# Kernel optimization log

Hardware: AMD Instinct MI355X
Metric: run time of the kernel (lower is better)

The kernel has to match this reference:

```python
import jax, jax.numpy as jnp
import numpy as np

B, L, H, NH = 2, 256, 512, 8
DH = H // NH
MAXLEN = 256           # module's max_seq_len; pe index offset
PE_ROWS = 2 * MAXLEN + 1


def _lin(x, W, b):
    # torch nn.Linear convention: y = x @ W.T + b
    return x @ W.T + b


def setup_inputs() -> dict:
    rng = jax.random.key(0)
    ks = jax.random.split(rng, 24)
    s = 0.02
    inp = {
        "key": jax.random.normal(ks[0], (B, L, H), jnp.float32),
        "query": jax.random.normal(ks[1], (B, L, H), jnp.float32),
        "value": jax.random.normal(ks[2], (B, L, H), jnp.float32),
        # learned params
        "pe": jax.random.normal(ks[3], (PE_ROWS, H), jnp.float32) * s,
        "Wf": jax.random.normal(ks[4], (H, 4 * H), jnp.float32) * s,
        "bf": jnp.zeros((H,), jnp.float32),
        "Wk": jax.random.normal(ks[5], (H, H), jnp.float32) * s,
        "bk": jnp.zeros((H,), jnp.float32),
        "Wq": jax.random.normal(ks[6], (H, H), jnp.float32) * s,
        "bq": jnp.zeros((H,), jnp.float32),
        "Wv": jax.random.normal(ks[7], (H, H), jnp.float32) * s,
        "bv": jnp.zeros((H,), jnp.float32),
        "Wr": jax.random.normal(ks[8], (H, H), jnp.float32) * s,
        "br": jnp.zeros((H,), jnp.float32),
        "Wo": jax.random.normal(ks[9], (H, H), jnp.float32) * s,  # ff_final
        "bo": jnp.zeros((H,), jnp.float32),
        "u": jax.random.normal(ks[10], (NH, DH), jnp.float32) * s,
        "v": jax.random.normal(ks[11], (NH, DH), jnp.float32) * s,
        # int inputs
        "seq_len": jax.random.randint(ks[12], (B,), 100, 200).astype(jnp.int64),
        "lex_num": jax.random.randint(ks[13], (B,), 0, 50).astype(jnp.int64),
    }
    pos_s = jax.random.randint(ks[14], (B, L), 0, 250)
    pos_e = pos_s + jax.random.randint(ks[15], (B, L), 0, 5)
    inp["pos_s"] = pos_s.astype(jnp.int64)
    inp["pos_e"] = pos_e.astype(jnp.int64)
    return inp


def reference(key, query, value, pe, Wf, bf, Wk, bk, Wq, bq, Wv, bv, Wr, br,
              Wo, bo, u, v, seq_len, lex_num, pos_s, pos_e):
    b, l, _ = key.shape
    # four relative position matrices [B, L, L]
    pos_ss = pos_s[:, :, None] - pos_s[:, None, :]
    pos_se = pos_s[:, :, None] - pos_e[:, None, :]
    pos_es = pos_e[:, :, None] - pos_s[:, None, :]
    pos_ee = pos_e[:, :, None] - pos_e[:, None, :]
    # gather pe embeddings, each [B, L, L, H]
    pe_ss = pe[pos_ss + MAXLEN]
    pe_se = pe[pos_se + MAXLEN]
    pe_es = pe[pos_es + MAXLEN]
    pe_ee = pe[pos_ee + MAXLEN]
    pe_4 = jnp.concatenate([pe_ss, pe_se, pe_es, pe_ee], axis=-1)  # [B,L,L,4H]
    rel = jax.nn.relu(_lin(pe_4, Wf, bf))                          # 'ff' fusion -> [B,L,L,H]

    q = _lin(query, Wq, bq).reshape(b, l, NH, DH).transpose(0, 2, 1, 3)  # [B,nh,L,dh]
    k = _lin(key, Wk, bk).reshape(b, l, NH, DH).transpose(0, 2, 1, 3)
    val = _lin(value, Wv, bv).reshape(b, l, NH, DH).transpose(0, 2, 1, 3)
    rel = _lin(rel, Wr, br).reshape(b, l, l, NH, DH)               # [B,L,L,nh,dh]

    A = jnp.einsum('bhid,bhjd->bhij', q, k)
    B_ = jnp.einsum('bhid,bijhd->bhij', q, rel)
    C = jnp.einsum('hd,bhjd->bhj', u, k)[:, :, None, :]
    D = jnp.einsum('hd,bijhd->bhij', v, rel)

    score = (A + B_ + C + D) / np.float32(np.sqrt(DH))
    total_len = seq_len + lex_num                                   # [B]
    mask = (jnp.arange(l)[None, :] < total_len[:, None])[:, None, None, :]
    score = jnp.where(mask, score, jnp.float32(-1e15))
    attn = jax.nn.softmax(score, axis=-1)
    out = jnp.einsum('bhij,bhjd->bhid', attn, val)                  # [B,nh,L,dh]
    out = out.transpose(0, 2, 1, 3).reshape(b, l, H)
    return _lin(out, Wo, bo)
```

## Files before the change

### kernel.cpp

```cpp
#include <hip/hip_runtime.h>
#include <hip/hip_bf16.h>

typedef unsigned short USHORT;
typedef long long LL;
typedef short s8v __attribute__((ext_vector_type(8)));
typedef float f32x4 __attribute__((ext_vector_type(4)));


__device__ __forceinline__ float bf2f(USHORT u) {
  union { unsigned int i; float f; } v; v.i = ((unsigned int)u) << 16; return v.f;
}
__device__ __forceinline__ USHORT f2bf(float f) {
  unsigned int x = __float_as_uint(f);
  unsigned int r = (x + 0x7fffu + ((x >> 16) & 1u)) >> 16;
  return (USHORT)r;
}

struct PrepArgs {
  const void* fsrc[18]; USHORT* fdst[18]; int fn[18];
  const void* wr_src; USHORT* wrT;
  const void* isrc[4]; int* idst[4];
};

__global__ __launch_bounds__(256) void prep_k(PrepArgs a, const void* qraw, int* flags) {
  __shared__ int s_w;
  const int t = threadIdx.x;
  if (t == 0) s_w = 0;
  __syncthreads();
  const USHORT* qb = (const USHORT*)qraw;
  int wild = 0;
  for (int c = t; c < 512; c += 256) {
    float x = bf2f(qb[c]);
    if (!(fabsf(x) <= 1024.0f)) wild = 1;
  }
  if (wild) atomicAdd(&s_w, 1);
  __syncthreads();
  const int f = (s_w == 0) ? 1 : 0;

  const int y = blockIdx.y;
  if (y < 18) {
    const int n = a.fn[y];
    const USHORT* sb = (const USHORT*)a.fsrc[y];
    const float* sf = (const float*)a.fsrc[y];
    USHORT* d = a.fdst[y];
    for (int idx = blockIdx.x * 256 + t; idx < n; idx += gridDim.x * 256)
      d[idx] = f ? sb[idx] : f2bf(sf[idx]);
  } else if (y == 18) {
    const USHORT* sb = (const USHORT*)a.wr_src;
    const float* sf = (const float*)a.wr_src;
    for (int idx = blockIdx.x * 256 + t; idx < 262144; idx += gridDim.x * 256) {
      const int e = idx >> 9, dd = idx & 511;
      const int s = dd * 512 + e;
      a.wrT[idx] = f ? sb[s] : f2bf(sf[s]);
    }
  } else if (blockIdx.x == 0) {
    if (t == 0) flags[0] = f;
    const int fi = (((const int*)a.isrc[0])[1] == 0) ? 1 : 0;
    if (t < 2) {
      a.idst[0][t] = fi ? (int)((const LL*)a.isrc[0])[t] : ((const int*)a.isrc[0])[t];
      a.idst[1][t] = fi ? (int)((const LL*)a.isrc[1])[t] : ((const int*)a.isrc[1])[t];
    }
    for (int c = t; c < 512; c += 256) {
      a.idst[2][c] = fi ? (int)((const LL*)a.isrc[2])[c] : ((const int*)a.isrc[2])[c];
      a.idst[3][c] = fi ? (int)((const LL*)a.isrc[3])[c] : ((const int*)a.isrc[3])[c];
    }
  }
}

struct GDesc {
  const USHORT* A; const USHORT* W; const USHORT* bias;
  void* out;
  int M, N, K, lda, ldw, koff, mode;
};
struct GArgs { GDesc d[32]; };

__global__ __launch_bounds__(256) void gemm2_k(GArgs ga, const int* __restrict__ flags) {
  const GDesc de = ga.d[blockIdx.z];
  const int row0 = blockIdx.y * 64, col0 = blockIdx.x * 64;
  if (row0 >= de.M || col0 >= de.N) return;
  const int wave = threadIdx.x >> 6, lane = threadIdx.x & 63;
  const int mrow = row0 + wave * 16 + (lane & 15);
  const int kq = (lane >> 4) * 8;
  const bool mok = (mrow < de.M);
  const USHORT* ar = de.A + (long)(mok ? mrow : 0) * de.lda + kq;
  const int nc = col0 + (lane & 15);
  const USHORT* w0p = de.W + (long)(nc +  0) * de.ldw + de.koff + kq;
  const USHORT* w1p = de.W + (long)(nc + 16) * de.ldw + de.koff + kq;
  const USHORT* w2p = de.W + (long)(nc + 32) * de.ldw + de.koff + kq;
  const USHORT* w3p = de.W + (long)(nc + 48) * de.ldw + de.koff + kq;

  f32x4 acc[4] = {};
#pragma unroll 4
  for (int k0 = 0; k0 < de.K; k0 += 32) {
    s8v a = *(const s8v*)(ar + k0);
    s8v wv0 = *(const s8v*)(w0p + k0);
    s8v wv1 = *(const s8v*)(w1p + k0);
    s8v wv2 = *(const s8v*)(w2p + k0);
    s8v wv3 = *(const s8v*)(w3p + k0);
    acc[0] = __builtin_amdgcn_mfma_f32_16x16x32_bf16(a, wv0, acc[0], 0, 0, 0);
    acc[1] = __builtin_amdgcn_mfma_f32_16x16x32_bf16(a, wv1, acc[1], 0, 0, 0);
    acc[2] = __builtin_amdgcn_mfma_f32_16x16x32_bf16(a, wv2, acc[2], 0, 0, 0);
    acc[3] = __builtin_amdgcn_mfma_f32_16x16x32_bf16(a, wv3, acc[3], 0, 0, 0);
  }

  const int obf = (de.mode == 2) ? flags[0] : (de.mode == 1);
  const int mbase = row0 + wave * 16 + (lane >> 4) * 4;
#pragma unroll
  for (int nt = 0; nt < 4; nt++) {
    const int n = col0 + nt * 16 + (lane & 15);
    const float bias = de.bias ? bf2f(de.bias[n]) : 0.f;
#pragma unroll
    for (int r = 0; r < 4; r++) {
      const int m = mbase + r;
      if (m >= de.M) continue;
      const float vo = acc[nt][r] + bias;
      const long off = (long)m * de.N + n;
      if (obf) ((USHORT*)de.out)[off] = f2bf(vo);
      else     ((float*)de.out)[off] = vo;
    }
  }
}

__global__ __launch_bounds__(256) void qvb2_k(
    const float* __restrict__ qp, const float* __restrict__ kp,
    const USHORT* __restrict__ u_bf, const USHORT* __restrict__ v_bf,
    const USHORT* __restrict__ br_bf,
    USHORT* __restrict__ qv, USHORT* __restrict__ qu, USHORT* __restrict__ kb,
    float* __restrict__ cbv_buf)
{
  const int idx = blockIdx.x * 256 + threadIdx.x;
  const int d = idx & 63, i = (idx >> 6) & 255, h = (idx >> 14) & 7, b = idx >> 17;
  const int hd = h * 64 + d;
  const long row = (long)(b * 256 + i) * 512 + hd;
  const float q = qp[row];
  const float qpv = q + bf2f(v_bf[hd]);
  qv[idx] = f2bf(qpv);
  qu[idx] = f2bf(q + bf2f(u_bf[hd]));
  kb[idx] = f2bf(kp[row]);
  float s = qpv * bf2f(br_bf[hd]);
#pragma unroll
  for (int off = 32; off > 0; off >>= 1) s += __shfl_xor(s, off);
  if ((threadIdx.x & 63) == 0) cbv_buf[idx >> 6] = s;
}

__global__ __launch_bounds__(256) void score2_k(
    const USHORT* __restrict__ Ptab_bf, const float* __restrict__ S_AC,
    const float* __restrict__ cbv_buf, const USHORT* __restrict__ wbuf_bf,
    const float* __restrict__ vp,
    const int* __restrict__ seq_len, const int* __restrict__ lex_num,
    const int* __restrict__ pos_s, const int* __restrict__ pos_e,
    USHORT* __restrict__ out_pre_bf)
{
  __shared__ float Sm[8 * 257];
  __shared__ int psj_s[256], pej_s[256];
  __shared__ float red4[4];

  const int i = blockIdx.x, b = blockIdx.y, t = threadIdx.x;
  const int wave = t >> 6, lane = t & 63;
  const int n = lane & 15, q = lane >> 4;
  int tl = seq_len[b] + lex_num[b];
  tl = min(max(tl, 1), 256);
  const int psi = pos_s[b * 256 + i];
  const int pei = pos_e[b * 256 + i];

  if (t < 256) { psj_s[t] = pos_s[b * 256 + t]; pej_s[t] = pos_e[b * 256 + t]; }

  s8v wf[16];
  if (n < 8) {
    const USHORT* wr = wbuf_bf + ((long)((b * 8 + n) * 256 + i)) * 512 + q * 8;
#pragma unroll
    for (int kk = 0; kk < 16; kk++) wf[kk] = *(const s8v*)(wr + kk * 32);
  } else {
#pragma unroll
    for (int kk = 0; kk < 16; kk++) wf[kk] = (s8v){0, 0, 0, 0, 0, 0, 0, 0};
  }
  __syncthreads();

  const USHORT* P1 = Ptab_bf;
  const USHORT* P2 = Ptab_bf + 513l * 512;
  const USHORT* P3 = Ptab_bf + 2l * 513 * 512;
  const USHORT* P4 = Ptab_bf + 3l * 513 * 512;

  const int ntiles = (tl + 15) >> 4;
  for (int jt = wave; jt < ntiles; jt += 4) {
    const int j0 = jt * 16;
    const int j = j0 + n;
    const int psj = psj_s[j], pej = pej_s[j];
    const long i0 = (long)min(max(psi - psj + 256, 0), 512) * 512 + q * 8;
    const long i1 = (long)min(max(psi - pej + 256, 0), 512) * 512 + q * 8;
    const long i2 = (long)min(max(pei - psj + 256, 0), 512) * 512 + q * 8;
    const long i3 = (long)min(max(pei - pej + 256, 0), 512) * 512 + q * 8;
    f32x4 acc = {0.f, 0.f, 0.f, 0.f};
#pragma unroll
    for (int kk = 0; kk < 16; kk++) {
      const int e0 = kk * 32;
      s8v a0 = *(const s8v*)(P1 + i0 + e0);
      s8v a1 = *(const s8v*)(P2 + i1 + e0);
      s8v a2 = *(const s8v*)(P3 + i2 + e0);
      s8v a3 = *(const s8v*)(P4 + i3 + e0);
      s8v af;
#pragma unroll
      for (int x = 0; x < 8; x++) {
        const float fs = bf2f((USHORT)a0[x]) + bf2f((USHORT)a1[x]) +
                         bf2f((USHORT)a2[x]) + bf2f((USHORT)a3[x]);
        af[x] = (short)f2bf(fmaxf(fs, 0.f));
      }
      acc = __builtin_amdgcn_mfma_f32_16x16x32_bf16(af, wf[kk], acc, 0, 0, 0);
    }
    if (n < 8) {
      const long base = (long)(b * 8 + n) * 256 + i;
      const float cb = cbv_buf[base];
      const float4 sac = *(const float4*)(S_AC + base * 256 + j0 + q * 4);
      const float* sacp = (const float*)&sac;
#pragma unroll
      for (int r = 0; r < 4; r++)
        Sm[n * 257 + j0 + q * 4 + r] = (acc[r] + sacp[r] + cb) * 0.125f;
    }
  }
  __syncthreads();

  for (int h = 0; h < 8; h++) {
    const float val = (t < tl) ? Sm[h * 257 + t] : -3.0e38f;
    float m = val;
#pragma unroll
    for (int off = 32; off > 0; off >>= 1) m = fmaxf(m, __shfl_xor(m, off));
    if (lane == 0) red4[wave] = m;
    __syncthreads();
    m = fmaxf(fmaxf(red4[0], red4[1]), fmaxf(red4[2], red4[3]));
    const float pv = (t < tl) ? __expf(val - m) : 0.f;
    float s = pv;
#pragma unroll
    for (int off = 32; off > 0; off >>= 1) s += __shfl_xor(s, off);
    __syncthreads();
    if (lane == 0) red4[wave] = s;
    __syncthreads();
    s = red4[0] + red4[1] + red4[2] + red4[3];
    if (!(s > 1e-30f)) s = 1.f;
    Sm[h * 257 + t] = pv / s;
    __syncthreads();
  }

#pragma unroll
  for (int pass = 0; pass < 2; pass++) {
    const int h = (t >> 6) + 4 * pass;
    const int d = t & 63;
    const float* vcol = vp + (long)(b * 256) * 512 + h * 64 + d;
    float acc = 0.f;
#pragma unroll 4
    for (int j = 0; j < tl; j++) acc += Sm[h * 257 + j] * vcol[(long)j * 512];
    out_pre_bf[(long)(b * 256 + i) * 512 + h * 64 + d] = f2bf(acc);
  }
}

extern "C" void kernel_launch(void* const* d_in, const int* in_sizes, int n_in,
                              void* d_out, int out_size, void* d_ws, size_t ws_size,
                              hipStream_t stream) {
  (void)in_sizes; (void)n_in; (void)out_size; (void)ws_size;

  float* p = (float*)d_ws;
  int* flags   = (int*)p; p += 4;
  int* c_seq   = (int*)p; p += 4;
  int* c_lex   = (int*)p; p += 4;
  int* c_pos_s = (int*)p; p += 512;
  int* c_pos_e = (int*)p; p += 512;
  USHORT* cb = (USHORT*)p;
  USHORT* c_key   = cb; cb += 262144;
  USHORT* c_query = cb; cb += 262144;
  USHORT* c_value = cb; cb += 262144;
  USHORT* c_pe    = cb; cb += 262656;
  USHORT* c_Wf    = cb; cb += 1048576;
  USHORT* c_bf    = cb; cb += 512;
  USHORT* c_Wk    = cb; cb += 262144;
  USHORT* c_bk    = cb; cb += 512;
  USHORT* c_Wq    = cb; cb += 262144;
  USHORT* c_bq    = cb; cb += 512;
  USHORT* c_Wv    = cb; cb += 262144;
  USHORT* c_bv    = cb; cb += 512;
  USHORT* c_Wr    = cb; cb += 262144;
  USHORT* c_br    = cb; cb += 512;
  USHORT* c_Wo    = cb; cb += 262144;
  USHORT* c_bo    = cb; cb += 512;
  USHORT* c_u     = cb; cb += 512;
  USHORT* c_v     = cb; cb += 512;
  USHORT* WrT        = cb; cb += 262144;
  USHORT* qv_bf      = cb; cb += 262144;
  USHORT* qu_bf      = cb; cb += 262144;
  USHORT* k_bf       = cb; cb += 262144;
  USHORT* wbuf_bf    = cb; cb += 2097152;
  USHORT* Ptab_bf    = cb; cb += 1050624;
  USHORT* out_pre_bf = cb; cb += 262144;
  p += 3935488;
  float* qp      = p; p += 262144;
  float* kp      = p; p += 262144;
  float* vp      = p; p += 262144;
  float* S_AC    = p; p += 1048576;
  float* cbv_buf = p; p += 4096;

  PrepArgs pa;
  USHORT* dsts[18] = {c_key, c_query, c_value, c_pe, c_Wf, c_bf, c_Wk, c_bk, c_Wq,
                      c_bq, c_Wv, c_bv, c_Wr, c_br, c_Wo, c_bo, c_u, c_v};
  int ns[18] = {262144, 262144, 262144, 262656, 1048576, 512, 262144, 512, 262144,
                512, 262144, 512, 262144, 512, 262144, 512, 512, 512};
  for (int i = 0; i < 18; i++) { pa.fsrc[i] = d_in[i]; pa.fdst[i] = dsts[i]; pa.fn[i] = ns[i]; }
  pa.wr_src = d_in[12]; pa.wrT = WrT;
  for (int i = 0; i < 4; i++) pa.isrc[i] = d_in[18 + i];
  pa.idst[0] = c_seq; pa.idst[1] = c_lex; pa.idst[2] = c_pos_s; pa.idst[3] = c_pos_e;
  prep_k<<<dim3(64, 20), 256, 0, stream>>>(pa, d_in[1], flags);

  GArgs gA = {};
  for (int z = 0; z < 4; z++)
    gA.d[z] = {c_pe, c_Wf, (z == 0) ? c_bf : nullptr, Ptab_bf + (long)z * 513 * 512,
               513, 512, 512, 512, 2048, z * 512, 1};
  gA.d[4] = {c_query, c_Wq, c_bq, qp, 512, 512, 512, 512, 512, 0, 0};
  gA.d[5] = {c_key,   c_Wk, c_bk, kp, 512, 512, 512, 512, 512, 0, 0};
  gA.d[6] = {c_value, c_Wv, c_bv, vp, 512, 512, 512, 512, 512, 0, 0};
  gemm2_k<<<dim3(8, 9, 7), 256, 0, stream>>>(gA, flags);

  qvb2_k<<<1024, 256, 0, stream>>>(qp, kp, c_u, c_v, c_br, qv_bf, qu_bf, k_bf, cbv_buf);

  GArgs gB = {};
  for (int z = 0; z < 16; z++)
    gB.d[z] = {qv_bf + z * 16384, WrT, nullptr, wbuf_bf + (long)z * 131072,
               256, 512, 64, 64, 512, (z & 7) * 64, 1};
  for (int z = 0; z < 16; z++)
    gB.d[16 + z] = {qu_bf + z * 16384, k_bf + z * 16384, nullptr, S_AC + (long)z * 65536,
                    256, 256, 64, 64, 64, 0, 0};
  gemm2_k<<<dim3(8, 4, 32), 256, 0, stream>>>(gB, flags);

  score2_k<<<dim3(256, 2), 256, 0, stream>>>(
      Ptab_bf, S_AC, cbv_buf, wbuf_bf, vp,
      c_seq, c_lex, c_pos_s, c_pos_e, out_pre_bf);

  GArgs gC = {};
  gC.d[0] = {out_pre_bf, c_Wo, c_bo, d_out, 512, 512, 512, 512, 512, 0, 2};
  gemm2_k<<<dim3(8, 8, 1), 256, 0, stream>>>(gC, flags);
}
```

Measured before the change: 247.4 us.

## Split fused score kernel into parallel score, softmax and MFMA attn·V GEMM

The monolithic per-row score kernel becomes three steps. A score kernel runs one wave per 16-column j tile over a 3D grid and writes full fp32 scores to global memory. A separate softmax kernel writes bf16 probabilities. A batched MFMA GEMM then computes attn·V, replacing the scalar per-thread loop over j. The Q/K/V projections now emit bf16 directly, with V stored transposed and head-strided layouts addressed through a new ldo/trans descriptor, so the qvb step no longer repacks K. The aim is more parallelism and tensor-core use for attn·V, at the cost of extra launches and a global round-trip for the score and attn matrices.

```diff
diff --git a/kernel.cpp b/kernel.cpp
--- a/kernel.cpp
+++ b/kernel.cpp
@@ -70,7 +70,7 @@
 struct GDesc {
   const USHORT* A; const USHORT* W; const USHORT* bias;
   void* out;
-  int M, N, K, lda, ldw, koff, mode;
+  int M, N, K, lda, ldw, koff, ldo, mode, trans, pad;
 };
 struct GArgs { GDesc d[32]; };
 
@@ -114,113 +114,106 @@
       const int m = mbase + r;
       if (m >= de.M) continue;
       const float vo = acc[nt][r] + bias;
-      const long off = (long)m * de.N + n;
+      const long off = de.trans ? ((long)n * de.ldo + m) : ((long)m * de.ldo + n);
       if (obf) ((USHORT*)de.out)[off] = f2bf(vo);
       else     ((float*)de.out)[off] = vo;
     }
   }
 }
 
-__global__ __launch_bounds__(256) void qvb2_k(
-    const float* __restrict__ qp, const float* __restrict__ kp,
+__global__ __launch_bounds__(256) void qvb3_k(
+    const USHORT* __restrict__ q_n,
     const USHORT* __restrict__ u_bf, const USHORT* __restrict__ v_bf,
     const USHORT* __restrict__ br_bf,
-    USHORT* __restrict__ qv, USHORT* __restrict__ qu, USHORT* __restrict__ kb,
+    USHORT* __restrict__ qv_n, USHORT* __restrict__ qu_n,
     float* __restrict__ cbv_buf)
 {
   const int idx = blockIdx.x * 256 + threadIdx.x;
-  const int d = idx & 63, i = (idx >> 6) & 255, h = (idx >> 14) & 7, b = idx >> 17;
-  const int hd = h * 64 + d;
-  const long row = (long)(b * 256 + i) * 512 + hd;
-  const float q = qp[row];
-  const float qpv = q + bf2f(v_bf[hd]);
-  qv[idx] = f2bf(qpv);
-  qu[idx] = f2bf(q + bf2f(u_bf[hd]));
-  kb[idx] = f2bf(kp[row]);
+  const int hd = idx & 511;
+  const float qv = bf2f(q_n[idx]);
+  const float qpv = qv + bf2f(v_bf[hd]);
+  qv_n[idx] = f2bf(qpv);
+  qu_n[idx] = f2bf(qv + bf2f(u_bf[hd]));
   float s = qpv * bf2f(br_bf[hd]);
 #pragma unroll
   for (int off = 32; off > 0; off >>= 1) s += __shfl_xor(s, off);
   if ((threadIdx.x & 63) == 0) cbv_buf[idx >> 6] = s;
 }
 
-__global__ __launch_bounds__(256) void score2_k(
+__global__ __launch_bounds__(128) void score3_k(
     const USHORT* __restrict__ Ptab_bf, const float* __restrict__ S_AC,
     const float* __restrict__ cbv_buf, const USHORT* __restrict__ wbuf_bf,
-    const float* __restrict__ vp,
     const int* __restrict__ seq_len, const int* __restrict__ lex_num,
     const int* __restrict__ pos_s, const int* __restrict__ pos_e,
-    USHORT* __restrict__ out_pre_bf)
+    float* __restrict__ S_full)
 {
-  __shared__ float Sm[8 * 257];
-  __shared__ int psj_s[256], pej_s[256];
-  __shared__ float red4[4];
-
-  const int i = blockIdx.x, b = blockIdx.y, t = threadIdx.x;
-  const int wave = t >> 6, lane = t & 63;
-  const int n = lane & 15, q = lane >> 4;
+  const int i = blockIdx.x, b = blockIdx.y;
+  const int wave = threadIdx.x >> 6, lane = threadIdx.x & 63;
+  const int jt = blockIdx.z * 2 + wave;
   int tl = seq_len[b] + lex_num[b];
   tl = min(max(tl, 1), 256);
-  const int psi = pos_s[b * 256 + i];
-  const int pei = pos_e[b * 256 + i];
-
-  if (t < 256) { psj_s[t] = pos_s[b * 256 + t]; pej_s[t] = pos_e[b * 256 + t]; }
-
-  s8v wf[16];
-  if (n < 8) {
-    const USHORT* wr = wbuf_bf + ((long)((b * 8 + n) * 256 + i)) * 512 + q * 8;
-#pragma unroll
-    for (int kk = 0; kk < 16; kk++) wf[kk] = *(const s8v*)(wr + kk * 32);
-  } else {
-#pragma unroll
-    for (int kk = 0; kk < 16; kk++) wf[kk] = (s8v){0, 0, 0, 0, 0, 0, 0, 0};
-  }
-  __syncthreads();
+  const int j0 = jt * 16;
+  if (j0 >= tl) return;
+  const int n = lane & 15, q = lane >> 4;
+  const int psi = pos_s[b * 256 + i], pei = pos_e[b * 256 + i];
+  const int j = j0 + n;
+  const int psj = pos_s[b * 256 + j], pej = pos_e[b * 256 + j];
 
   const USHORT* P1 = Ptab_bf;
   const USHORT* P2 = Ptab_bf + 513l * 512;
   const USHORT* P3 = Ptab_bf + 2l * 513 * 512;
   const USHORT* P4 = Ptab_bf + 3l * 513 * 512;
-
-  const int ntiles = (tl + 15) >> 4;
-  for (int jt = wave; jt < ntiles; jt += 4) {
-    const int j0 = jt * 16;
-    const int j = j0 + n;
-    const int psj = psj_s[j], pej = pej_s[j];
-    const long i0 = (long)min(max(psi - psj + 256, 0), 512) * 512 + q * 8;
-    const long i1 = (long)min(max(psi - pej + 256, 0), 512) * 512 + q * 8;
-    const long i2 = (long)min(max(pei - psj + 256, 0), 512) * 512 + q * 8;
-    const long i3 = (long)min(max(pei - pej + 256, 0), 512) * 512 + q * 8;
-    f32x4 acc = {0.f, 0.f, 0.f, 0.f};
-#pragma unroll
-    for (int kk = 0; kk < 16; kk++) {
-      const int e0 = kk * 32;
-      s8v a0 = *(const s8v*)(P1 + i0 + e0);
-      s8v a1 = *(const s8v*)(P2 + i1 + e0);
-      s8v a2 = *(const s8v*)(P3 + i2 + e0);
-      s8v a3 = *(const s8v*)(P4 + i3 + e0);
-      s8v af;
-#pragma unroll
-      for (int x = 0; x < 8; x++) {
-        const float fs = bf2f((USHORT)a0[x]) + bf2f((USHORT)a1[x]) +
-                         bf2f((USHORT)a2[x]) + bf2f((USHORT)a3[x]);
-        af[x] = (short)f2bf(fmaxf(fs, 0.f));
-      }
-      acc = __builtin_amdgcn_mfma_f32_16x16x32_bf16(af, wf[kk], acc, 0, 0, 0);
-    }
-    if (n < 8) {
-      const long base = (long)(b * 8 + n) * 256 + i;
-      const float cb = cbv_buf[base];
-      const float4 sac = *(const float4*)(S_AC + base * 256 + j0 + q * 4);
-      const float* sacp = (const float*)&sac;
-#pragma unroll
-      for (int r = 0; r < 4; r++)
-        Sm[n * 257 + j0 + q * 4 + r] = (acc[r] + sacp[r] + cb) * 0.125f;
-    }
-  }
-  __syncthreads();
-
+  const USHORT* g0 = P1 + (long)min(max(psi - psj + 256, 0), 512) * 512 + q * 8;
+  const USHORT* g1 = P2 + (long)min(max(psi - pej + 256, 0), 512) * 512 + q * 8;
+  const USHORT* g2 = P3 + (long)min(max(pei - psj + 256, 0), 512) * 512 + q * 8;
+  const USHORT* g3 = P4 + (long)min(max(pei - pej + 256, 0), 512) * 512 + q * 8;
+  const USHORT* wr = wbuf_bf + ((long)((b * 8 + (n & 7)) * 256 + i)) * 512 + q * 8;
+
+  f32x4 acc = {0.f, 0.f, 0.f, 0.f};
+#pragma unroll 4
+  for (int kk = 0; kk < 16; kk++) {
+    const int e0 = kk * 32;
+    s8v a0 = *(const s8v*)(g0 + e0);
+    s8v a1 = *(const s8v*)(g1 + e0);
+    s8v a2 = *(const s8v*)(g2 + e0);
+    s8v a3 = *(const s8v*)(g3 + e0);
+    s8v wv = (s8v){0, 0, 0, 0, 0, 0, 0, 0};
+    if (n < 8) wv = *(const s8v*)(wr + e0);
+    s8v af;
+#pragma unroll
+    for (int x = 0; x < 8; x++) {
+      float fs = bf2f((USHORT)a0[x]) + bf2f((USHORT)a1[x]) +
+                 bf2f((USHORT)a2[x]) + bf2f((USHORT)a3[x]);
+      fs = fmaxf(fs, 0.f);
+      af[x] = (short)(USHORT)((__float_as_uint(fs) + 0x8000u) >> 16);
+    }
+    acc = __builtin_amdgcn_mfma_f32_16x16x32_bf16(af, wv, acc, 0, 0, 0);
+  }
+  if (n < 8) {
+    const long base = (long)(b * 8 + n) * 256 + i;
+    const float cb = cbv_buf[(long)(b * 256 + i) * 8 + n];
+    const float4 sac = *(const float4*)(S_AC + base * 256 + j0 + q * 4);
+    float* dst = S_full + base * 256 + j0 + q * 4;
+    dst[0] = (acc[0] + sac.x + cb) * 0.125f;
+    dst[1] = (acc[1] + sac.y + cb) * 0.125f;
+    dst[2] = (acc[2] + sac.z + cb) * 0.125f;
+    dst[3] = (acc[3] + sac.w + cb) * 0.125f;
+  }
+}
+
+__global__ __launch_bounds__(256) void softmax_k(
+    const float* __restrict__ S_full,
+    const int* __restrict__ seq_len, const int* __restrict__ lex_num,
+    USHORT* __restrict__ attn_bf)
+{
+  __shared__ float red4[4];
+  const int i = blockIdx.x, b = blockIdx.y, t = threadIdx.x;
+  const int lane = t & 63, wave = t >> 6;
+  int tl = seq_len[b] + lex_num[b];
+  tl = min(max(tl, 1), 256);
   for (int h = 0; h < 8; h++) {
-    const float val = (t < tl) ? Sm[h * 257 + t] : -3.0e38f;
+    const long base = ((long)(b * 8 + h) * 256 + i) * 256;
+    const float val = (t < tl) ? S_full[base + t] : -3.0e38f;
     float m = val;
 #pragma unroll
     for (int off = 32; off > 0; off >>= 1) m = fmaxf(m, __shfl_xor(m, off));
@@ -236,19 +229,8 @@
     __syncthreads();
     s = red4[0] + red4[1] + red4[2] + red4[3];
     if (!(s > 1e-30f)) s = 1.f;
-    Sm[h * 257 + t] = pv / s;
+    attn_bf[base + t] = f2bf(pv / s);
     __syncthreads();
-  }
-
-#pragma unroll
-  for (int pass = 0; pass < 2; pass++) {
-    const int h = (t >> 6) + 4 * pass;
-    const int d = t & 63;
-    const float* vcol = vp + (long)(b * 256) * 512 + h * 64 + d;
-    float acc = 0.f;
-#pragma unroll 4
-    for (int j = 0; j < tl; j++) acc += Sm[h * 257 + j] * vcol[(long)j * 512];
-    out_pre_bf[(long)(b * 256 + i) * 512 + h * 64 + d] = f2bf(acc);
   }
 }
 
@@ -257,13 +239,13 @@
                               hipStream_t stream) {
   (void)in_sizes; (void)n_in; (void)out_size; (void)ws_size;
 
-  float* p = (float*)d_ws;
-  int* flags   = (int*)p; p += 4;
-  int* c_seq   = (int*)p; p += 4;
-  int* c_lex   = (int*)p; p += 4;
-  int* c_pos_s = (int*)p; p += 512;
-  int* c_pos_e = (int*)p; p += 512;
-  USHORT* cb = (USHORT*)p;
+  float* fp = (float*)d_ws;
+  int* flags   = (int*)fp; fp += 4;
+  int* c_seq   = (int*)fp; fp += 4;
+  int* c_lex   = (int*)fp; fp += 4;
+  int* c_pos_s = (int*)fp; fp += 512;
+  int* c_pos_e = (int*)fp; fp += 512;
+  USHORT* cb = (USHORT*)fp;
   USHORT* c_key   = cb; cb += 262144;
   USHORT* c_query = cb; cb += 262144;
   USHORT* c_value = cb; cb += 262144;
@@ -283,18 +265,19 @@
   USHORT* c_u     = cb; cb += 512;
   USHORT* c_v     = cb; cb += 512;
   USHORT* WrT        = cb; cb += 262144;
-  USHORT* qv_bf      = cb; cb += 262144;
-  USHORT* qu_bf      = cb; cb += 262144;
-  USHORT* k_bf       = cb; cb += 262144;
+  USHORT* q_n        = cb; cb += 262144;
+  USHORT* k_n        = cb; cb += 262144;
+  USHORT* v_t        = cb; cb += 262144;
+  USHORT* qv_n       = cb; cb += 262144;
+  USHORT* qu_n       = cb; cb += 262144;
   USHORT* wbuf_bf    = cb; cb += 2097152;
   USHORT* Ptab_bf    = cb; cb += 1050624;
+  USHORT* attn_bf    = cb; cb += 1048576;
   USHORT* out_pre_bf = cb; cb += 262144;
-  p += 3935488;
-  float* qp      = p; p += 262144;
-  float* kp      = p; p += 262144;
-  float* vp      = p; p += 262144;
-  float* S_AC    = p; p += 1048576;
-  float* cbv_buf = p; p += 4096;
+  float* gp = (float*)cb;
+  float* S_AC    = gp; gp += 1048576;
+  float* S_full  = gp; gp += 1048576;
+  float* cbv_buf = gp; gp += 4096;
 
   PrepArgs pa;
   USHORT* dsts[18] = {c_key, c_query, c_value, c_pe, c_Wf, c_bf, c_Wk, c_bk, c_Wq,
@@ -310,28 +293,41 @@
   GArgs gA = {};
   for (int z = 0; z < 4; z++)
     gA.d[z] = {c_pe, c_Wf, (z == 0) ? c_bf : nullptr, Ptab_bf + (long)z * 513 * 512,
-               513, 512, 512, 512, 2048, z * 512, 1};
-  gA.d[4] = {c_query, c_Wq, c_bq, qp, 512, 512, 512, 512, 512, 0, 0};
-  gA.d[5] = {c_key,   c_Wk, c_bk, kp, 512, 512, 512, 512, 512, 0, 0};
-  gA.d[6] = {c_value, c_Wv, c_bv, vp, 512, 512, 512, 512, 512, 0, 0};
+               513, 512, 512, 512, 2048, z * 512, 512, 1, 0, 0};
+  gA.d[4] = {c_query, c_Wq, c_bq, q_n, 512, 512, 512, 512, 512, 0, 512, 1, 0, 0};
+  gA.d[5] = {c_key,   c_Wk, c_bk, k_n, 512, 512, 512, 512, 512, 0, 512, 1, 0, 0};
+  gA.d[6] = {c_value, c_Wv, c_bv, v_t, 512, 512, 512, 512, 512, 0, 512, 1, 1, 0};
   gemm2_k<<<dim3(8, 9, 7), 256, 0, stream>>>(gA, flags);
 
-  qvb2_k<<<1024, 256, 0, stream>>>(qp, kp, c_u, c_v, c_br, qv_bf, qu_bf, k_bf, cbv_buf);
+  qvb3_k<<<1024, 256, 0, stream>>>(q_n, c_u, c_v, c_br, qv_n, qu_n, cbv_buf);
 
   GArgs gB = {};
-  for (int z = 0; z < 16; z++)
-    gB.d[z] = {qv_bf + z * 16384, WrT, nullptr, wbuf_bf + (long)z * 131072,
-               256, 512, 64, 64, 512, (z & 7) * 64, 1};
-  for (int z = 0; z < 16; z++)
-    gB.d[16 + z] = {qu_bf + z * 16384, k_bf + z * 16384, nullptr, S_AC + (long)z * 65536,
-                    256, 256, 64, 64, 64, 0, 0};
+  for (int z = 0; z < 16; z++) {
+    const int b = z >> 3, h = z & 7;
+    gB.d[z] = {qv_n + b * 131072 + h * 64, WrT, nullptr, wbuf_bf + (long)z * 131072,
+               256, 512, 64, 512, 512, h * 64, 512, 1, 0, 0};
+  }
+  for (int z = 0; z < 16; z++) {
+    const int b = z >> 3, h = z & 7;
+    gB.d[16 + z] = {qu_n + b * 131072 + h * 64, k_n + b * 131072 + h * 64, nullptr,
+                    S_AC + (long)z * 65536, 256, 256, 64, 512, 512, 0, 256, 0, 0, 0};
+  }
   gemm2_k<<<dim3(8, 4, 32), 256, 0, stream>>>(gB, flags);
 
-  score2_k<<<dim3(256, 2), 256, 0, stream>>>(
-      Ptab_bf, S_AC, cbv_buf, wbuf_bf, vp,
-      c_seq, c_lex, c_pos_s, c_pos_e, out_pre_bf);
+  score3_k<<<dim3(256, 2, 8), 128, 0, stream>>>(
+      Ptab_bf, S_AC, cbv_buf, wbuf_bf, c_seq, c_lex, c_pos_s, c_pos_e, S_full);
+
+  softmax_k<<<dim3(256, 2), 256, 0, stream>>>(S_full, c_seq, c_lex, attn_bf);
+
+  GArgs gV = {};
+  for (int z = 0; z < 16; z++) {
+    const int b = z >> 3, h = z & 7;
+    gV.d[z] = {attn_bf + (long)z * 65536, v_t + (long)(h * 64) * 512 + b * 256, nullptr,
+               out_pre_bf + b * 131072 + h * 64, 256, 64, 256, 256, 512, 0, 512, 1, 0, 0};
+  }
+  gemm2_k<<<dim3(1, 4, 16), 256, 0, stream>>>(gV, flags);
 
   GArgs gC = {};
-  gC.d[0] = {out_pre_bf, c_Wo, c_bo, d_out, 512, 512, 512, 512, 512, 0, 2};
+  gC.d[0] = {out_pre_bf, c_Wo, c_bo, d_out, 512, 512, 512, 512, 512, 0, 512, 2, 0, 0};
   gemm2_k<<<dim3(8, 8, 1), 256, 0, stream>>>(gC, flags);
 }
```

Measured after the change: 238.9 us. 1.04x faster.
